# Kernel optimization log

Hardware: AMD Instinct MI355X
Metric: run time of the kernel (lower is better)

## Reference

```python
import jax, jax.numpy as jnp
import numpy as np

BATCH = 2048
INPUT_DIM = 512
N = 8 ** 4  # reservoir_n ** reservoir_d = 4096
T = 16
NEG_SLOPE = 0.1
SPARSITY = 0.1  # fraction of nonzero entries in the pre-trained reservoir W


def setup_inputs() -> dict:
    key = jax.random.key(0)
    kx, kw, km = jax.random.split(key, 3)
    x = jax.random.normal(kx, (BATCH, INPUT_DIM), dtype=jnp.float32)
    # Sparse pre-trained reservoir weights; scale keeps spectral norm ~O(1)
    # so the T-step recurrence neither explodes nor vanishes.
    mask = (jax.random.uniform(km, (N, N)) < SPARSITY).astype(jnp.float32)
    W = jax.random.normal(kw, (N, N), dtype=jnp.float32) * mask / jnp.sqrt(SPARSITY * N)
    return {"x": x, "W": W}


def reference(x, W):
    # Pad input [B, input_dim] -> initial state S [B, N]
    S0 = jnp.pad(x, ((0, 0), (0, N - x.shape[1])))

    def step(S, _):
        S = jax.nn.leaky_relu(S @ W, negative_slope=NEG_SLOPE)
        return S, None

    S_final, _ = jax.lax.scan(step, S0, None, length=T)
    return S_final
```

## Files before the change

kernel.cpp:

```cpp
#include <hip/hip_runtime.h>


#define BATCH 2048
#define NDIM  4096
#define INDIM 512
#define BM 128
#define BN 128
#define BK 32

typedef _Float16 f16x8 __attribute__((ext_vector_type(8)));
typedef float    f32x4 __attribute__((ext_vector_type(4)));

__device__ __forceinline__ void async16(const void* gsrc, void* ldst) {
  const __attribute__((address_space(1))) unsigned int* g =
      (const __attribute__((address_space(1))) unsigned int*)gsrc;
  __attribute__((address_space(3))) unsigned int* l =
      (__attribute__((address_space(3))) unsigned int*)ldst;
  __builtin_amdgcn_global_load_lds(g, l, 16, 0, 0);
}

__global__ void prep_x(const float* __restrict__ x,
                       _Float16* __restrict__ Sh, _Float16* __restrict__ Sl) {
  size_t i = (size_t)blockIdx.x * 256 + threadIdx.x;
  int b = (int)(i >> 12);
  int n = (int)(i & (NDIM - 1));
  float v = (n < INDIM) ? x[(size_t)b * INDIM + n] : 0.0f;
  _Float16 h = (_Float16)v;
  Sh[i] = h;
  Sl[i] = (_Float16)(v - (float)h);
}

__global__ void prep_w(const float* __restrict__ W,
                       _Float16* __restrict__ Wth, _Float16* __restrict__ Wtl) {
  __shared__ float tile[32][33];
  int k0 = blockIdx.y * 32, n0 = blockIdx.x * 32;
  int tx = threadIdx.x, ty = threadIdx.y;
  for (int r = 0; r < 4; r++) {
    int k = k0 + ty + r * 8;
    tile[ty + r * 8][tx] = W[(size_t)k * NDIM + n0 + tx];
  }
  __syncthreads();
  for (int r = 0; r < 4; r++) {
    int n = n0 + ty + r * 8;
    float v = tile[tx][ty + r * 8] * 256.0f;
    _Float16 h = (_Float16)v;
    Wth[(size_t)n * NDIM + k0 + tx] = h;
    Wtl[(size_t)n * NDIM + k0 + tx] = (_Float16)(v - (float)h);
  }
}

#define READF(b, A, L, Bv, M)                          \
  do {                                                 \
    _Pragma("unroll") for (int i = 0; i < 4; i++) {    \
      A[i]  = *(const f16x8*)&sAh[b][oA[i]];           \
      L[i]  = *(const f16x8*)&sAl[b][oA[i]];           \
      Bv[i] = *(const f16x8*)&sBh[b][oB[i]];           \
      M[i]  = *(const f16x8*)&sBl[b][oB[i]];           \
    }                                                  \
  } while (0)

#define MFMAS(A, L, Bv, M)                                                          \
  do {                                                                              \
    _Pragma("unroll") for (int j = 0; j < 4; j++)                                   \
    _Pragma("unroll") for (int i = 0; i < 4; i++) {                                 \
      acc[i][j] = __builtin_amdgcn_mfma_f32_16x16x32_f16(A[i], Bv[j], acc[i][j], 0, 0, 0); \
      acc[i][j] = __builtin_amdgcn_mfma_f32_16x16x32_f16(L[i], Bv[j], acc[i][j], 0, 0, 0); \
      acc[i][j] = __builtin_amdgcn_mfma_f32_16x16x32_f16(A[i], M[j], acc[i][j], 0, 0, 0); \
    }                                                                               \
  } while (0)

template <int MODE>
__global__ __launch_bounds__(256, 2) void step_kernel(
    const _Float16* __restrict__ Ah, const _Float16* __restrict__ Al,
    const _Float16* __restrict__ Bh, const _Float16* __restrict__ Bl,
    _Float16* __restrict__ Dh, _Float16* __restrict__ Dl,
    float* __restrict__ Dout, int k_len) {
  __shared__ _Float16 sAh[2][BM * BK];
  __shared__ _Float16 sAl[2][BM * BK];
  __shared__ _Float16 sBh[2][BN * BK];
  __shared__ _Float16 sBl[2][BN * BK];

  const int tid = threadIdx.x;
  const int lane = tid & 63;
  const int w = tid >> 6;
  const int wm = w >> 1, wn = w & 1;

  int id = blockIdx.x;
  int xcd = id & 7, local = id >> 3;
  int lr = local & 7, lc = local >> 3;
  const int bm = ((xcd & 1) * 8 + lr) * BM;
  const int bn = ((xcd >> 1) * 8 + lc) * BN;

  const int sr = lane >> 2, cl = lane & 3;
  const int fm = lane & 15, fq = lane >> 4;

  int oA[4], oB[4];
#pragma unroll
  for (int i = 0; i < 4; i++) {
    int rA = wm * 64 + i * 16 + fm;
    oA[i] = rA * BK + (fq ^ ((rA >> 1) & 3)) * 8;
    int rB = wn * 64 + i * 16 + fm;
    oB[i] = rB * BK + (fq ^ ((rB >> 1) & 3)) * 8;
  }

  int r0 = w * 32 + sr, r1 = r0 + 16;
  int cg0 = cl ^ ((r0 >> 1) & 3);
  int cg1 = cl ^ ((r1 >> 1) & 3);
  const size_t gA0 = (size_t)(bm + r0) * NDIM + cg0 * 8;
  const size_t gA1 = (size_t)(bm + r1) * NDIM + cg1 * 8;
  const size_t gB0 = (size_t)(bn + r0) * NDIM + cg0 * 8;
  const size_t gB1 = (size_t)(bn + r1) * NDIM + cg1 * 8;
  const int lo0 = r0 * BK + cl * 8;
  const int lo1 = r1 * BK + cl * 8;

  auto stage = [&](int kt, int b) {
    async16(Ah + gA0 + kt, &sAh[b][lo0]);
    async16(Ah + gA1 + kt, &sAh[b][lo1]);
    async16(Al + gA0 + kt, &sAl[b][lo0]);
    async16(Al + gA1 + kt, &sAl[b][lo1]);
    async16(Bh + gB0 + kt, &sBh[b][lo0]);
    async16(Bh + gB1 + kt, &sBh[b][lo1]);
    async16(Bl + gB0 + kt, &sBl[b][lo0]);
    async16(Bl + gB1 + kt, &sBl[b][lo1]);
  };

  f32x4 acc[4][4];
#pragma unroll
  for (int i = 0; i < 4; i++)
#pragma unroll
    for (int j = 0; j < 4; j++) acc[i][j] = (f32x4){0.f, 0.f, 0.f, 0.f};

  f16x8 a0[4], l0[4], b0[4], m0[4];
  f16x8 a1[4], l1[4], b1[4], m1[4];

  const int nk = k_len / BK;

  stage(0 * BK, 0);
  stage(1 * BK, 1);
  __syncthreads();
  READF(0, a0, l0, b0, m0);
  __syncthreads();
  stage(2 * BK, 0);

  int it = 1;
  for (; it + 1 < nk; it += 2) {
    READF(1, a1, l1, b1, m1);
    MFMAS(a0, l0, b0, m0);
    __syncthreads();
    if (it + 2 < nk) stage((it + 2) * BK, 1);

    READF(0, a0, l0, b0, m0);
    MFMAS(a1, l1, b1, m1);
    __syncthreads();
    if (it + 3 < nk) stage((it + 3) * BK, 0);
  }
  READF(1, a1, l1, b1, m1);
  MFMAS(a0, l0, b0, m0);
  MFMAS(a1, l1, b1, m1);

  const float inv = 1.0f / 256.0f;
#pragma unroll
  for (int i = 0; i < 4; i++) {
#pragma unroll
    for (int j = 0; j < 4; j++) {
#pragma unroll
      for (int e = 0; e < 4; e++) {
        int r = bm + wm * 64 + i * 16 + fq * 4 + e;
        int c = bn + wn * 64 + j * 16 + fm;
        float g = acc[i][j][e] * inv;
        float s = (g > 0.0f) ? g : 0.1f * g;
        if (MODE == 0) {
          _Float16 h = (_Float16)s;
          Dh[(size_t)r * NDIM + c] = h;
          Dl[(size_t)r * NDIM + c] = (_Float16)(s - (float)h);
        } else {
          Dout[(size_t)r * NDIM + c] = s;
        }
      }
    }
  }
}

extern "C" void kernel_launch(void* const* d_in, const int* in_sizes, int n_in,
                              void* d_out, int out_size, void* d_ws, size_t ws_size,
                              hipStream_t stream) {
  const float* x = (const float*)d_in[0];
  const float* W = (const float*)d_in[1];
  float* out = (float*)d_out;
  char* ws = (char*)d_ws;

  const size_t WT_BYTES = (size_t)NDIM * NDIM * 2;
  const size_t S_BYTES = (size_t)BATCH * NDIM * 2;
  _Float16* Wth = (_Float16*)ws;
  _Float16* Wtl = (_Float16*)(ws + WT_BYTES);
  _Float16* SAh = (_Float16*)(ws + 2 * WT_BYTES);
  _Float16* SAl = (_Float16*)(ws + 2 * WT_BYTES + S_BYTES);
  _Float16* SBh = (_Float16*)(ws + 2 * WT_BYTES + 2 * S_BYTES);
  _Float16* SBl = (_Float16*)(ws + 2 * WT_BYTES + 3 * S_BYTES);

  prep_x<<<(BATCH * NDIM) / 256, 256, 0, stream>>>(x, SAh, SAl);
  prep_w<<<dim3(NDIM / 32, NDIM / 32), dim3(32, 8), 0, stream>>>(W, Wth, Wtl);

  dim3 grid((NDIM / BN) * (BATCH / BM));
  for (int t = 1; t <= 16; t++) {
    const _Float16* ah = (t & 1) ? SAh : SBh;
    const _Float16* al = (t & 1) ? SAl : SBl;
    _Float16* dh = (t & 1) ? SBh : SAh;
    _Float16* dl = (t & 1) ? SBl : SAl;
    int klen = (t == 1) ? INDIM : NDIM;
    if (t < 16)
      step_kernel<0><<<grid, 256, 0, stream>>>(ah, al, Wth, Wtl, dh, dl, nullptr, klen);
    else
      step_kernel<1><<<grid, 256, 0, stream>>>(ah, al, Wth, Wtl, nullptr, nullptr, out, klen);
  }
}
```

Before: 2.415 ms.

## Switch to 32x32x16 MFMA and load A fragments directly from global

Replaces the 16x16x32 MFMA tiling with 32x32x16 MFMA tiles, so each wave does fewer, larger matrix instructions. The A operand (state hi/lo) is no longer staged through LDS; each lane reads its fragments straight from global memory into registers, double-buffered across k-steps, while only B (weights) stays in LDS. This halves LDS traffic and footprint and may improve occupancy. The cost is uncoalesced, latency-exposed global reads for A with less cross-wave reuse, since the two waves sharing a row block each fetch it.

Measured after the change: 4.657 ms. +92.8%, slower.

```diff
diff --git a/kernel.cpp b/kernel.cpp
--- a/kernel.cpp
+++ b/kernel.cpp
@@ -8,8 +8,8 @@
 #define BN 128
 #define BK 32
 
-typedef _Float16 f16x8 __attribute__((ext_vector_type(8)));
-typedef float    f32x4 __attribute__((ext_vector_type(4)));
+typedef _Float16 f16x8  __attribute__((ext_vector_type(8)));
+typedef float    f32x16 __attribute__((ext_vector_type(16)));
 
 __device__ __forceinline__ void async16(const void* gsrc, void* ldst) {
   const __attribute__((address_space(1))) unsigned int* g =
@@ -49,24 +49,33 @@
   }
 }
 
-#define READF(b, A, L, Bv, M)                          \
-  do {                                                 \
-    _Pragma("unroll") for (int i = 0; i < 4; i++) {    \
-      A[i]  = *(const f16x8*)&sAh[b][oA[i]];           \
-      L[i]  = *(const f16x8*)&sAl[b][oA[i]];           \
-      Bv[i] = *(const f16x8*)&sBh[b][oB[i]];           \
-      M[i]  = *(const f16x8*)&sBl[b][oB[i]];           \
-    }                                                  \
+#define LOADA(kt, AH, AL)                                    \
+  do {                                                       \
+    _Pragma("unroll") for (int i = 0; i < 2; i++)            \
+    _Pragma("unroll") for (int s = 0; s < 2; s++) {          \
+      AH[i][s] = *(const f16x8*)(Ah + gA[i] + (kt) + s * 16);\
+      AL[i][s] = *(const f16x8*)(Al + gA[i] + (kt) + s * 16);\
+    }                                                        \
   } while (0)
 
-#define MFMAS(A, L, Bv, M)                                                          \
-  do {                                                                              \
-    _Pragma("unroll") for (int j = 0; j < 4; j++)                                   \
-    _Pragma("unroll") for (int i = 0; i < 4; i++) {                                 \
-      acc[i][j] = __builtin_amdgcn_mfma_f32_16x16x32_f16(A[i], Bv[j], acc[i][j], 0, 0, 0); \
-      acc[i][j] = __builtin_amdgcn_mfma_f32_16x16x32_f16(L[i], Bv[j], acc[i][j], 0, 0, 0); \
-      acc[i][j] = __builtin_amdgcn_mfma_f32_16x16x32_f16(A[i], M[j], acc[i][j], 0, 0, 0); \
-    }                                                                               \
+#define READB(b)                                             \
+  do {                                                       \
+    _Pragma("unroll") for (int j = 0; j < 2; j++)            \
+    _Pragma("unroll") for (int s = 0; s < 2; s++) {          \
+      bh[j][s] = *(const f16x8*)&sBh[b][oB[j][s]];           \
+      bl[j][s] = *(const f16x8*)&sBl[b][oB[j][s]];           \
+    }                                                        \
+  } while (0)
+
+#define MFMAS(AH, AL)                                                                        \
+  do {                                                                                       \
+    _Pragma("unroll") for (int j = 0; j < 2; j++)                                            \
+    _Pragma("unroll") for (int i = 0; i < 2; i++)                                            \
+    _Pragma("unroll") for (int s = 0; s < 2; s++) {                                          \
+      acc[i][j] = __builtin_amdgcn_mfma_f32_32x32x16_f16(AH[i][s], bh[j][s], acc[i][j], 0, 0, 0); \
+      acc[i][j] = __builtin_amdgcn_mfma_f32_32x32x16_f16(AL[i][s], bh[j][s], acc[i][j], 0, 0, 0); \
+      acc[i][j] = __builtin_amdgcn_mfma_f32_32x32x16_f16(AH[i][s], bl[j][s], acc[i][j], 0, 0, 0); \
+    }                                                                                        \
   } while (0)
 
 template <int MODE>
@@ -75,8 +84,6 @@
     const _Float16* __restrict__ Bh, const _Float16* __restrict__ Bl,
     _Float16* __restrict__ Dh, _Float16* __restrict__ Dl,
     float* __restrict__ Dout, int k_len) {
-  __shared__ _Float16 sAh[2][BM * BK];
-  __shared__ _Float16 sAl[2][BM * BK];
   __shared__ _Float16 sBh[2][BN * BK];
   __shared__ _Float16 sBl[2][BN * BK];
 
@@ -91,82 +98,78 @@
   const int bm = ((xcd & 1) * 8 + lr) * BM;
   const int bn = ((xcd >> 1) * 8 + lc) * BN;
 
+  const int l31 = lane & 31, l5 = lane >> 5;
+
+  int oB[2][2];
+#pragma unroll
+  for (int j = 0; j < 2; j++)
+#pragma unroll
+    for (int s = 0; s < 2; s++) {
+      int row = wn * 64 + j * 32 + l31;
+      int c = s * 2 + l5;
+      oB[j][s] = row * BK + (c ^ ((row >> 1) & 3)) * 8;
+    }
+
+  size_t gA[2];
+#pragma unroll
+  for (int i = 0; i < 2; i++)
+    gA[i] = (size_t)(bm + wm * 64 + i * 32 + l31) * NDIM + l5 * 8;
+
   const int sr = lane >> 2, cl = lane & 3;
-  const int fm = lane & 15, fq = lane >> 4;
-
-  int oA[4], oB[4];
-#pragma unroll
-  for (int i = 0; i < 4; i++) {
-    int rA = wm * 64 + i * 16 + fm;
-    oA[i] = rA * BK + (fq ^ ((rA >> 1) & 3)) * 8;
-    int rB = wn * 64 + i * 16 + fm;
-    oB[i] = rB * BK + (fq ^ ((rB >> 1) & 3)) * 8;
-  }
-
-  int r0 = w * 32 + sr, r1 = r0 + 16;
-  int cg0 = cl ^ ((r0 >> 1) & 3);
-  int cg1 = cl ^ ((r1 >> 1) & 3);
-  const size_t gA0 = (size_t)(bm + r0) * NDIM + cg0 * 8;
-  const size_t gA1 = (size_t)(bm + r1) * NDIM + cg1 * 8;
+  const int r0 = w * 32 + sr, r1 = r0 + 16;
+  const int cg0 = cl ^ ((r0 >> 1) & 3), cg1 = cl ^ ((r1 >> 1) & 3);
   const size_t gB0 = (size_t)(bn + r0) * NDIM + cg0 * 8;
   const size_t gB1 = (size_t)(bn + r1) * NDIM + cg1 * 8;
-  const int lo0 = r0 * BK + cl * 8;
-  const int lo1 = r1 * BK + cl * 8;
-
-  auto stage = [&](int kt, int b) {
-    async16(Ah + gA0 + kt, &sAh[b][lo0]);
-    async16(Ah + gA1 + kt, &sAh[b][lo1]);
-    async16(Al + gA0 + kt, &sAl[b][lo0]);
-    async16(Al + gA1 + kt, &sAl[b][lo1]);
+  const int lo0 = r0 * BK + cl * 8, lo1 = r1 * BK + cl * 8;
+
+  auto stageB = [&](int kt, int b) {
     async16(Bh + gB0 + kt, &sBh[b][lo0]);
     async16(Bh + gB1 + kt, &sBh[b][lo1]);
     async16(Bl + gB0 + kt, &sBl[b][lo0]);
     async16(Bl + gB1 + kt, &sBl[b][lo1]);
   };
 
-  f32x4 acc[4][4];
-#pragma unroll
-  for (int i = 0; i < 4; i++)
-#pragma unroll
-    for (int j = 0; j < 4; j++) acc[i][j] = (f32x4){0.f, 0.f, 0.f, 0.f};
-
-  f16x8 a0[4], l0[4], b0[4], m0[4];
-  f16x8 a1[4], l1[4], b1[4], m1[4];
+  f32x16 acc[2][2];
+#pragma unroll
+  for (int i = 0; i < 2; i++)
+#pragma unroll
+    for (int j = 0; j < 2; j++)
+#pragma unroll
+      for (int e = 0; e < 16; e++) acc[i][j][e] = 0.0f;
+
+  f16x8 a0h[2][2], a0l[2][2], a1h[2][2], a1l[2][2];
+  f16x8 bh[2][2], bl[2][2];
 
   const int nk = k_len / BK;
 
-  stage(0 * BK, 0);
-  stage(1 * BK, 1);
+  stageB(0, 0);
+  stageB(BK, 1);
+  LOADA(0, a0h, a0l);
   __syncthreads();
-  READF(0, a0, l0, b0, m0);
-  __syncthreads();
-  stage(2 * BK, 0);
-
-  int it = 1;
-  for (; it + 1 < nk; it += 2) {
-    READF(1, a1, l1, b1, m1);
-    MFMAS(a0, l0, b0, m0);
+
+  for (int it = 0; it < nk; it += 2) {
+    READB(0);
+    LOADA((it + 1) * BK, a1h, a1l);
+    MFMAS(a0h, a0l);
     __syncthreads();
-    if (it + 2 < nk) stage((it + 2) * BK, 1);
-
-    READF(0, a0, l0, b0, m0);
-    MFMAS(a1, l1, b1, m1);
+    if (it + 2 < nk) stageB((it + 2) * BK, 0);
+
+    READB(1);
+    if (it + 2 < nk) LOADA((it + 2) * BK, a0h, a0l);
+    MFMAS(a1h, a1l);
     __syncthreads();
-    if (it + 3 < nk) stage((it + 3) * BK, 0);
-  }
-  READF(1, a1, l1, b1, m1);
-  MFMAS(a0, l0, b0, m0);
-  MFMAS(a1, l1, b1, m1);
+    if (it + 3 < nk) stageB((it + 3) * BK, 1);
+  }
 
   const float inv = 1.0f / 256.0f;
 #pragma unroll
-  for (int i = 0; i < 4; i++) {
-#pragma unroll
-    for (int j = 0; j < 4; j++) {
-#pragma unroll
-      for (int e = 0; e < 4; e++) {
-        int r = bm + wm * 64 + i * 16 + fq * 4 + e;
-        int c = bn + wn * 64 + j * 16 + fm;
+  for (int i = 0; i < 2; i++) {
+#pragma unroll
+    for (int j = 0; j < 2; j++) {
+#pragma unroll
+      for (int e = 0; e < 16; e++) {
+        int r = bm + wm * 64 + i * 32 + (e & 3) + 8 * (e >> 2) + 4 * l5;
+        int c = bn + wn * 64 + j * 32 + l31;
         float g = acc[i][j][e] * inv;
         float s = (g > 0.0f) ? g : 0.1f * g;
         if (MODE == 0) {
```

## Load MFMA fragments directly from global memory, dropping LDS staging

Applied to the files above, without the earlier changes.

Removes the shared-memory double buffer fed by async global-to-LDS copies and the barriers around it. Each wave now reads its MFMA operand fragments straight from global memory into registers, using two register sets as a software prefetch. This avoids LDS traffic and synchronisation, but every wave re-reads A and B tiles that other waves also use. It relies on L1/L2 to absorb that redundancy, and the 16-byte-per-lane row-strided accesses coalesce poorly.

Measured after the change: 7.230 ms. +199.4%, slower.

```diff
diff --git a/kernel.cpp b/kernel.cpp
--- a/kernel.cpp
+++ b/kernel.cpp
@@ -10,14 +10,6 @@
 
 typedef _Float16 f16x8 __attribute__((ext_vector_type(8)));
 typedef float    f32x4 __attribute__((ext_vector_type(4)));
-
-__device__ __forceinline__ void async16(const void* gsrc, void* ldst) {
-  const __attribute__((address_space(1))) unsigned int* g =
-      (const __attribute__((address_space(1))) unsigned int*)gsrc;
-  __attribute__((address_space(3))) unsigned int* l =
-      (__attribute__((address_space(3))) unsigned int*)ldst;
-  __builtin_amdgcn_global_load_lds(g, l, 16, 0, 0);
-}
 
 __global__ void prep_x(const float* __restrict__ x,
                        _Float16* __restrict__ Sh, _Float16* __restrict__ Sl) {
@@ -49,24 +41,24 @@
   }
 }
 
-#define READF(b, A, L, Bv, M)                          \
+#define LOADF(kt, A, L, Bv, M)                         \
   do {                                                 \
     _Pragma("unroll") for (int i = 0; i < 4; i++) {    \
-      A[i]  = *(const f16x8*)&sAh[b][oA[i]];           \
-      L[i]  = *(const f16x8*)&sAl[b][oA[i]];           \
-      Bv[i] = *(const f16x8*)&sBh[b][oB[i]];           \
-      M[i]  = *(const f16x8*)&sBl[b][oB[i]];           \
+      A[i]  = *(const f16x8*)(Ah + oA[i] + (kt));      \
+      L[i]  = *(const f16x8*)(Al + oA[i] + (kt));      \
+      Bv[i] = *(const f16x8*)(Bh + oB[i] + (kt));      \
+      M[i]  = *(const f16x8*)(Bl + oB[i] + (kt));      \
     }                                                  \
   } while (0)
 
-#define MFMAS(A, L, Bv, M)                                                          \
-  do {                                                                              \
-    _Pragma("unroll") for (int j = 0; j < 4; j++)                                   \
-    _Pragma("unroll") for (int i = 0; i < 4; i++) {                                 \
+#define MFMAS(A, L, Bv, M)                                                                 \
+  do {                                                                                     \
+    _Pragma("unroll") for (int j = 0; j < 4; j++)                                          \
+    _Pragma("unroll") for (int i = 0; i < 4; i++) {                                        \
       acc[i][j] = __builtin_amdgcn_mfma_f32_16x16x32_f16(A[i], Bv[j], acc[i][j], 0, 0, 0); \
       acc[i][j] = __builtin_amdgcn_mfma_f32_16x16x32_f16(L[i], Bv[j], acc[i][j], 0, 0, 0); \
-      acc[i][j] = __builtin_amdgcn_mfma_f32_16x16x32_f16(A[i], M[j], acc[i][j], 0, 0, 0); \
-    }                                                                               \
+      acc[i][j] = __builtin_amdgcn_mfma_f32_16x16x32_f16(A[i], M[j], acc[i][j], 0, 0, 0);  \
+    }                                                                                      \
   } while (0)
 
 template <int MODE>
@@ -75,11 +67,6 @@
     const _Float16* __restrict__ Bh, const _Float16* __restrict__ Bl,
     _Float16* __restrict__ Dh, _Float16* __restrict__ Dl,
     float* __restrict__ Dout, int k_len) {
-  __shared__ _Float16 sAh[2][BM * BK];
-  __shared__ _Float16 sAl[2][BM * BK];
-  __shared__ _Float16 sBh[2][BN * BK];
-  __shared__ _Float16 sBl[2][BN * BK];
-
   const int tid = threadIdx.x;
   const int lane = tid & 63;
   const int w = tid >> 6;
@@ -91,38 +78,14 @@
   const int bm = ((xcd & 1) * 8 + lr) * BM;
   const int bn = ((xcd >> 1) * 8 + lc) * BN;
 
-  const int sr = lane >> 2, cl = lane & 3;
   const int fm = lane & 15, fq = lane >> 4;
 
-  int oA[4], oB[4];
+  size_t oA[4], oB[4];
 #pragma unroll
   for (int i = 0; i < 4; i++) {
-    int rA = wm * 64 + i * 16 + fm;
-    oA[i] = rA * BK + (fq ^ ((rA >> 1) & 3)) * 8;
-    int rB = wn * 64 + i * 16 + fm;
-    oB[i] = rB * BK + (fq ^ ((rB >> 1) & 3)) * 8;
+    oA[i] = (size_t)(bm + wm * 64 + i * 16 + fm) * NDIM + fq * 8;
+    oB[i] = (size_t)(bn + wn * 64 + i * 16 + fm) * NDIM + fq * 8;
   }
-
-  int r0 = w * 32 + sr, r1 = r0 + 16;
-  int cg0 = cl ^ ((r0 >> 1) & 3);
-  int cg1 = cl ^ ((r1 >> 1) & 3);
-  const size_t gA0 = (size_t)(bm + r0) * NDIM + cg0 * 8;
-  const size_t gA1 = (size_t)(bm + r1) * NDIM + cg1 * 8;
-  const size_t gB0 = (size_t)(bn + r0) * NDIM + cg0 * 8;
-  const size_t gB1 = (size_t)(bn + r1) * NDIM + cg1 * 8;
-  const int lo0 = r0 * BK + cl * 8;
-  const int lo1 = r1 * BK + cl * 8;
-
-  auto stage = [&](int kt, int b) {
-    async16(Ah + gA0 + kt, &sAh[b][lo0]);
-    async16(Ah + gA1 + kt, &sAh[b][lo1]);
-    async16(Al + gA0 + kt, &sAl[b][lo0]);
-    async16(Al + gA1 + kt, &sAl[b][lo1]);
-    async16(Bh + gB0 + kt, &sBh[b][lo0]);
-    async16(Bh + gB1 + kt, &sBh[b][lo1]);
-    async16(Bl + gB0 + kt, &sBl[b][lo0]);
-    async16(Bl + gB1 + kt, &sBl[b][lo1]);
-  };
 
   f32x4 acc[4][4];
 #pragma unroll
@@ -135,28 +98,13 @@
 
   const int nk = k_len / BK;
 
-  stage(0 * BK, 0);
-  stage(1 * BK, 1);
-  __syncthreads();
-  READF(0, a0, l0, b0, m0);
-  __syncthreads();
-  stage(2 * BK, 0);
-
-  int it = 1;
-  for (; it + 1 < nk; it += 2) {
-    READF(1, a1, l1, b1, m1);
+  LOADF(0, a0, l0, b0, m0);
+  for (int it = 0; it < nk; it += 2) {
+    LOADF((it + 1) * BK, a1, l1, b1, m1);
     MFMAS(a0, l0, b0, m0);
-    __syncthreads();
-    if (it + 2 < nk) stage((it + 2) * BK, 1);
-
-    READF(0, a0, l0, b0, m0);
+    if (it + 2 < nk) LOADF((it + 2) * BK, a0, l0, b0, m0);
     MFMAS(a1, l1, b1, m1);
-    __syncthreads();
-    if (it + 3 < nk) stage((it + 3) * BK, 0);
   }
-  READF(1, a1, l1, b1, m1);
-  MFMAS(a0, l0, b0, m0);
-  MFMAS(a1, l1, b1, m1);
 
   const float inv = 1.0f / 256.0f;
 #pragma unroll
```
